# Kernel optimization log

Hardware: AMD Instinct MI355X
Metric: run time of the kernel (lower is better)

The kernel has to match this reference:

```python
import jax, jax.numpy as jnp
import numpy as np

TAU = 0.28
EPS = 1e-08

def _l2norm(x):
    # F.normalize(dim=1): x / max(||x||, 1e-12)
    n = jnp.sqrt(jnp.sum(x * x, axis=1, keepdims=True))
    return x / jnp.maximum(n, 1e-12)

def setup_inputs() -> dict:
    key = jax.random.key(0)
    k1, k2 = jax.random.split(key)
    N, D = 16384, 64
    return {
        "user_embed": jax.random.normal(k1, (N, D), dtype=jnp.float32),
        "pos_item_embed": jax.random.normal(k2, (N, D), dtype=jnp.float32),
    }

def reference(user_embed, pos_item_embed):
    u = _l2norm(user_embed)          # [N, D]
    i = _l2norm(pos_item_embed)      # [N, D]
    pos_score = jnp.exp(jnp.sum(u * i, axis=-1) / TAU)          # [N]
    ui = jnp.matmul(u, i.T)          # [N, N]
    uu = jnp.matmul(u, u.T)          # [N, N]
    total = jnp.sum(jnp.exp((ui + uu) / TAU), axis=1)           # [N]
    na_loss = -jnp.log(pos_score / (total + EPS))
    return jnp.mean(na_loss)
```

## Files before the change

### kernel.cpp

```cpp
#include <hip/hip_runtime.h>
#include <hip/hip_bf16.h>

#define NROWS 16384
#define DIM 64
#define BCOLS 512
#define BROWS 1024
#define NCS (NROWS / BCOLS)
#define NRG (NROWS / BROWS)

static constexpr float TAU = 0.28f;
static constexpr float EPS = 1e-8f;
static constexpr float EXP2_SCALE = (float)(8388608.0 / (0.28 * 0.6931471805599453));
static constexpr int   EXPB = 1064870600;
static constexpr float LN2F = 0.69314718055994530942f;

using short8   = __attribute__((ext_vector_type(8))) short;
using f32x4    = __attribute__((ext_vector_type(4))) float;
using ushort4v = __attribute__((ext_vector_type(4))) unsigned short;

typedef __attribute__((address_space(1))) const unsigned char ga_t;
typedef __attribute__((address_space(3))) unsigned char la_t;

__global__ __launch_bounds__(256) void prep_kernel(
    const float* __restrict__ u, const float* __restrict__ v,
    __hip_bfloat16* __restrict__ a_out, __hip_bfloat16* __restrict__ w_out,
    float* __restrict__ p_out, float* __restrict__ total, float* __restrict__ out)
{
    const int lane = threadIdx.x & 63;
    const int wv   = threadIdx.x >> 6;
    const int l15  = lane & 15;
    const int row  = blockIdx.x * 16 + wv * 4 + (lane >> 4);

    const float4 uu = *(const float4*)(u + (size_t)row * DIM + l15 * 4);
    const float4 vv = *(const float4*)(v + (size_t)row * DIM + l15 * 4);

    float su = uu.x * uu.x + uu.y * uu.y + uu.z * uu.z + uu.w * uu.w;
    float si = vv.x * vv.x + vv.y * vv.y + vv.z * vv.z + vv.w * vv.w;
    float sd = uu.x * vv.x + uu.y * vv.y + uu.z * vv.z + uu.w * vv.w;
#pragma unroll
    for (int m = 1; m < 16; m <<= 1) {
        su += __shfl_xor(su, m, 64);
        si += __shfl_xor(si, m, 64);
        sd += __shfl_xor(sd, m, 64);
    }
    const float inv_u = 1.0f / fmaxf(sqrtf(su), 1e-12f);
    const float inv_i = 1.0f / fmaxf(sqrtf(si), 1e-12f);

    alignas(8) __hip_bfloat16 a4[4], w4[4];
    const float un[4] = {uu.x * inv_u, uu.y * inv_u, uu.z * inv_u, uu.w * inv_u};
    const float in[4] = {vv.x * inv_i, vv.y * inv_i, vv.z * inv_i, vv.w * inv_i};
#pragma unroll
    for (int r = 0; r < 4; r++) {
        a4[r] = __float2bfloat16(EXP2_SCALE * un[r]);
        w4[r] = __float2bfloat16(un[r] + in[r]);
    }
    *(ushort4v*)((unsigned short*)a_out + (size_t)row * DIM + l15 * 4) = *(ushort4v*)a4;
    *(ushort4v*)((unsigned short*)w_out + (size_t)row * DIM + l15 * 4) = *(ushort4v*)w4;

    if (l15 == 0) {
        p_out[row] = sd * inv_u * inv_i * (1.0f / TAU);
        total[row] = 0.0f;
    }
    if (blockIdx.x == 0 && threadIdx.x == 0) out[0] = 0.0f;
}

__global__ __launch_bounds__(512, 4) void score_kernel(
    const __hip_bfloat16* __restrict__ A, const __hip_bfloat16* __restrict__ W,
    float* __restrict__ total)
{
    __shared__ alignas(16) ushort blds[BCOLS * DIM];

    const int tid  = threadIdx.x;
    const int lane = tid & 63;
    const int wv   = tid >> 6;
    const int l15  = lane & 15;
    const int quad = lane >> 4;
    const int cs   = blockIdx.x & (NCS - 1);
    const int rg   = blockIdx.x >> 5;
    const int col0    = cs * BCOLS;
    const int rowbase = rg * BROWS;

    const ushort* Au = (const ushort*)A;
    const ushort* Wu = (const ushort*)W;

#pragma unroll
    for (int q = 0; q < 8; q++) {
        const int p = q * 512 + tid;
        const int j = p >> 3;
        const int c = (p & 7) ^ (j & 7);
        const ushort* g = Wu + (size_t)(col0 + j) * DIM + c * 8;
        __builtin_amdgcn_global_load_lds((ga_t*)g, (la_t*)&blds[(size_t)p * 8], 16, 0, 0);
    }
    __syncthreads();

#pragma unroll 1
    for (int si = 0; si < 2; si++) {
        const int r0 = rowbase + si * 512 + wv * 64;

        short8 af[4][2];
#pragma unroll
        for (int rs = 0; rs < 4; rs++)
#pragma unroll
            for (int kk = 0; kk < 2; kk++)
                af[rs][kk] = *(const short8*)(
                    Au + (size_t)(r0 + rs * 16 + l15) * DIM + kk * 32 + quad * 8);

        f32x4 rowsum[4];
#pragma unroll
        for (int rs = 0; rs < 4; rs++) rowsum[rs] = {0.f, 0.f, 0.f, 0.f};

#pragma unroll 4
        for (int ct = 0; ct < BCOLS / 16; ct++) {
            const int jl = ct * 16 + l15;
            const int sw = l15 & 7;
            const short8 b0 = *(const short8*)&blds[(size_t)(jl * 8 + (quad ^ sw)) * 8];
            const short8 b1 = *(const short8*)&blds[(size_t)(jl * 8 + ((4 + quad) ^ sw)) * 8];
#pragma unroll
            for (int rs = 0; rs < 4; rs++) {
                f32x4 acc = {0.f, 0.f, 0.f, 0.f};
                acc = __builtin_amdgcn_mfma_f32_16x16x32_bf16(af[rs][0], b0, acc, 0, 0, 0);
                acc = __builtin_amdgcn_mfma_f32_16x16x32_bf16(af[rs][1], b1, acc, 0, 0, 0);
#pragma unroll
                for (int r = 0; r < 4; r++)
                    rowsum[rs][r] += __int_as_float((int)acc[r] + EXPB);
            }
        }

#pragma unroll
        for (int m = 1; m < 16; m <<= 1)
#pragma unroll
            for (int rs = 0; rs < 4; rs++)
#pragma unroll
                for (int r = 0; r < 4; r++)
                    rowsum[rs][r] += __shfl_xor(rowsum[rs][r], m, 64);

        if (l15 == 0) {
#pragma unroll
            for (int rs = 0; rs < 4; rs++)
#pragma unroll
                for (int r = 0; r < 4; r++)
                    atomicAdd(&total[r0 + rs * 16 + quad * 4 + r], rowsum[rs][r]);
        }
    }
}

__global__ __launch_bounds__(256) void finalize_kernel(
    const float* __restrict__ total, const float* __restrict__ p,
    float* __restrict__ out)
{
    __shared__ float red[4];
    const int idx = blockIdx.x * 256 + threadIdx.x;
    float s = __log2f(total[idx] + EPS) * LN2F - p[idx];
#pragma unroll
    for (int m = 1; m < 64; m <<= 1) s += __shfl_xor(s, m, 64);
    if ((threadIdx.x & 63) == 0) red[threadIdx.x >> 6] = s;
    __syncthreads();
    if (threadIdx.x == 0)
        atomicAdd(out, (red[0] + red[1] + red[2] + red[3]) * (1.0f / (float)NROWS));
}

extern "C" void kernel_launch(void* const* d_in, const int* in_sizes, int n_in,
                              void* d_out, int out_size, void* d_ws, size_t ws_size,
                              hipStream_t stream) {
    const float* u = (const float*)d_in[0];
    const float* v = (const float*)d_in[1];

    char* ws = (char*)d_ws;
    __hip_bfloat16* a = (__hip_bfloat16*)(ws);
    __hip_bfloat16* w = (__hip_bfloat16*)(ws + (size_t)NROWS * DIM * 2);
    float* p   = (float*)(ws + (size_t)NROWS * DIM * 4);
    float* tot = (float*)(ws + (size_t)NROWS * DIM * 4 + (size_t)NROWS * 4);

    prep_kernel<<<NROWS / 16, 256, 0, stream>>>(u, v, a, w, p, tot, (float*)d_out);
    score_kernel<<<NRG * NCS, 512, 0, stream>>>(a, w, tot);
    finalize_kernel<<<NROWS / 256, 256, 0, stream>>>(tot, p, (float*)d_out);
}
```

Before: 103.1 us.

## Software-pipeline MFMA and exp accumulation with double-buffered accumulators

Restructures the inner column-tile loop into a two-stage software pipeline. MFMAs for one tile are issued while the exp-bit-trick accumulation of the previous tile runs, using two accumulator sets and sched_barriers to keep the compiler from reordering the stages. LDS loads for the next tile are also issued ahead. The goal is to overlap MFMA latency with VALU work, at the cost of more registers and disabling unroll 4, under a launch bound of 4 waves.

```diff
diff --git a/kernel.cpp b/kernel.cpp
--- a/kernel.cpp
+++ b/kernel.cpp
@@ -64,6 +64,29 @@
     if (blockIdx.x == 0 && threadIdx.x == 0) out[0] = 0.0f;
 }
 
+#define LOADB(ct, B0, B1) do {                                                 \
+    const int jl_ = (ct) * 16 + l15;                                           \
+    B0 = *(const short8*)&blds[(size_t)(jl_ * 8 + (quad ^ sw)) * 8];           \
+    B1 = *(const short8*)&blds[(size_t)(jl_ * 8 + ((4 + quad) ^ sw)) * 8];     \
+} while (0)
+
+#define MFMA4(ACC, B0, B1) do {                                                \
+    _Pragma("unroll")                                                          \
+    for (int rs_ = 0; rs_ < 4; rs_++) {                                        \
+        f32x4 t_ = {0.f, 0.f, 0.f, 0.f};                                       \
+        t_ = __builtin_amdgcn_mfma_f32_16x16x32_bf16(af[rs_][0], B0, t_, 0, 0, 0); \
+        ACC[rs_] = __builtin_amdgcn_mfma_f32_16x16x32_bf16(af[rs_][1], B1, t_, 0, 0, 0); \
+    }                                                                          \
+} while (0)
+
+#define EXP4(ACC) do {                                                         \
+    _Pragma("unroll")                                                          \
+    for (int rs_ = 0; rs_ < 4; rs_++)                                          \
+        _Pragma("unroll")                                                      \
+        for (int r_ = 0; r_ < 4; r_++)                                         \
+            rowsum[rs_][r_] += __int_as_float((int)ACC[rs_][r_] + EXPB);       \
+} while (0)
+
 __global__ __launch_bounds__(512, 4) void score_kernel(
     const __hip_bfloat16* __restrict__ A, const __hip_bfloat16* __restrict__ W,
     float* __restrict__ total)
@@ -75,6 +98,7 @@
     const int wv   = tid >> 6;
     const int l15  = lane & 15;
     const int quad = lane >> 4;
+    const int sw   = l15 & 7;
     const int cs   = blockIdx.x & (NCS - 1);
     const int rg   = blockIdx.x >> 5;
     const int col0    = cs * BCOLS;
@@ -85,11 +109,11 @@
 
 #pragma unroll
     for (int q = 0; q < 8; q++) {
-        const int p = q * 512 + tid;
-        const int j = p >> 3;
-        const int c = (p & 7) ^ (j & 7);
+        const int pp = q * 512 + tid;
+        const int j = pp >> 3;
+        const int c = (pp & 7) ^ (j & 7);
         const ushort* g = Wu + (size_t)(col0 + j) * DIM + c * 8;
-        __builtin_amdgcn_global_load_lds((ga_t*)g, (la_t*)&blds[(size_t)p * 8], 16, 0, 0);
+        __builtin_amdgcn_global_load_lds((ga_t*)g, (la_t*)&blds[(size_t)pp * 8], 16, 0, 0);
     }
     __syncthreads();
 
@@ -109,22 +133,29 @@
 #pragma unroll
         for (int rs = 0; rs < 4; rs++) rowsum[rs] = {0.f, 0.f, 0.f, 0.f};
 
-#pragma unroll 4
-        for (int ct = 0; ct < BCOLS / 16; ct++) {
-            const int jl = ct * 16 + l15;
-            const int sw = l15 & 7;
-            const short8 b0 = *(const short8*)&blds[(size_t)(jl * 8 + (quad ^ sw)) * 8];
-            const short8 b1 = *(const short8*)&blds[(size_t)(jl * 8 + ((4 + quad) ^ sw)) * 8];
-#pragma unroll
-            for (int rs = 0; rs < 4; rs++) {
-                f32x4 acc = {0.f, 0.f, 0.f, 0.f};
-                acc = __builtin_amdgcn_mfma_f32_16x16x32_bf16(af[rs][0], b0, acc, 0, 0, 0);
-                acc = __builtin_amdgcn_mfma_f32_16x16x32_bf16(af[rs][1], b1, acc, 0, 0, 0);
-#pragma unroll
-                for (int r = 0; r < 4; r++)
-                    rowsum[rs][r] += __int_as_float((int)acc[r] + EXPB);
-            }
+        short8 b0a, b1a, b0b, b1b;
+        f32x4 accA[4], accB[4];
+
+        LOADB(0, b0a, b1a);
+        LOADB(1, b0b, b1b);
+        MFMA4(accA, b0a, b1a);
+        __builtin_amdgcn_sched_barrier(0);
+
+#pragma unroll 1
+        for (int ct = 2; ct < BCOLS / 16; ct += 2) {
+            LOADB(ct, b0a, b1a);
+            MFMA4(accB, b0b, b1b);
+            __builtin_amdgcn_sched_barrier(0);
+            EXP4(accA);
+            LOADB(ct + 1, b0b, b1b);
+            MFMA4(accA, b0a, b1a);
+            __builtin_amdgcn_sched_barrier(0);
+            EXP4(accB);
         }
+        MFMA4(accB, b0b, b1b);
+        __builtin_amdgcn_sched_barrier(0);
+        EXP4(accA);
+        EXP4(accB);
 
 #pragma unroll
         for (int m = 1; m < 16; m <<= 1)
```

After: 106.1 us. 2.9% more time.
